# Kernel optimization log

Hardware: AMD Instinct MI355X
Metric: run time of the kernel (lower is better)

## Reference

```python
import jax, jax.numpy as jnp
import numpy as np

S, B, D = 4096, 4, 1024
APERTURE = 256
SCALE = 1.0 / np.sqrt(D)
EPS = 1e-6
NEG_INF = -jnp.inf


def _xavier(key, shape, gain=np.sqrt(2.0)):
    fan_in, fan_out = shape[1], shape[0]
    a = gain * np.sqrt(6.0 / (fan_in + fan_out))
    return jax.random.uniform(key, shape, jnp.float32, -a, a)


def setup_inputs() -> dict:
    key = jax.random.key(0)
    ks = jax.random.split(key, 8)
    return {
        "x": jax.random.normal(ks[0], (S, B, D), jnp.float32),
        "Wk": _xavier(ks[1], (D, D)),
        "Wq": _xavier(ks[2], (D, D)),
        "Wv": _xavier(ks[3], (D, D)),
        "Wp": _xavier(ks[4], (D, D)),
        "W1": _xavier(ks[5], (D, D)),
        "b1": jnp.full((D,), 0.1, jnp.float32),
        "W2": _xavier(ks[6], (1, D)),
        "b2": jnp.full((1,), 0.1, jnp.float32),
        "gamma": jnp.ones((D,), jnp.float32),
        "beta": jnp.zeros((D,), jnp.float32),
    }


def _layer_norm(y, gamma, beta):
    m = jnp.mean(y, axis=-1, keepdims=True)
    v = jnp.mean((y - m) ** 2, axis=-1, keepdims=True)
    return (y - m) * jax.lax.rsqrt(v + EPS) * gamma + beta


def reference(x, Wk, Wq, Wv, Wp, W1, b1, W2, b2, gamma, beta):
    # x: (S, B, D) -> (B, S, D)
    xb = jnp.transpose(x, (1, 0, 2))
    K = jnp.einsum('bsd,ed->bse', xb, Wk)
    Q = jnp.einsum('bsd,ed->bse', xb, Wq)
    V = jnp.einsum('bsd,ed->bse', xb, Wv)
    e = jnp.einsum('bqd,bkd->bqk', Q, K) * SCALE  # (B, S, S)
    # ignore_self: -inf on diagonal
    eye = jnp.eye(S, dtype=bool)
    e = jnp.where(eye[None, :, :], NEG_INF, e)
    # aperture mask: torch masks where tril(e,ap)*triu(e,-ap) == 0
    scope = jnp.tril(e, APERTURE) * jnp.triu(e, -APERTURE)
    e = jnp.where(scope == 0, NEG_INF, e)
    alpha = jax.nn.softmax(e, axis=2)  # dropout is identity at eval
    c = jnp.einsum('bqk,bkd->bqd', alpha, V)
    c = jnp.einsum('bqd,ed->bqe', c, Wp)
    y = c + xb
    y = _layer_norm(y, gamma, beta)
    y = jax.nn.relu(jnp.einsum('bsd,ed->bse', y, W1) + b1)
    y = _layer_norm(y, gamma, beta)
    y = jax.nn.sigmoid(jnp.einsum('bsd,ed->bse', y, W2) + b2)  # (B, S, 1)
    return jnp.transpose(y, (1, 0, 2))  # (S, B, 1)
```

## Files before the change

### kernel.cpp

```cpp
#include <hip/hip_runtime.h>
#include <stdint.h>
#include <math.h>

#define S_LEN 4096
#define BATCH 4
#define DIM   1024
#define AP    256
#define NBLK  32
#define BANDC 640
#define SCALE 0.03125f

typedef __attribute__((ext_vector_type(4))) float f32x4;
typedef __attribute__((ext_vector_type(8))) short bf16x8;

__device__ __forceinline__ ushort f2bf(float f) {
  union { float f; uint32_t u; } v; v.f = f;
  uint32_t r = v.u + 0x7FFFu + ((v.u >> 16) & 1u);
  return (ushort)(r >> 16);
}

__device__ __forceinline__ void gload16(const void* g, void* l) {
  __builtin_amdgcn_global_load_lds((const __attribute__((address_space(1))) void*)g,
                                   (__attribute__((address_space(3))) void*)l,
                                   16, 0, 0);
}

__device__ __forceinline__ float block_sum(float v, float* red) {
  #pragma unroll
  for (int o = 32; o > 0; o >>= 1) v += __shfl_xor(v, o, 64);
  const int w = threadIdx.x >> 6;
  if ((threadIdx.x & 63) == 0) red[w] = v;
  __syncthreads();
  v = red[0] + red[1] + red[2] + red[3];
  __syncthreads();
  return v;
}

__device__ __forceinline__ float block_max(float v, float* red) {
  #pragma unroll
  for (int o = 32; o > 0; o >>= 1) v = fmaxf(v, __shfl_xor(v, o, 64));
  const int w = threadIdx.x >> 6;
  if ((threadIdx.x & 63) == 0) red[w] = v;
  __syncthreads();
  v = fmaxf(fmaxf(red[0], red[1]), fmaxf(red[2], red[3]));
  __syncthreads();
  return v;
}

#define STAGE2(dstbase, g0, g1, kcol) \
  gload16((g0) + (kcol), lds + (dstbase) + stOff); \
  gload16((g1) + (kcol), lds + (dstbase) + 4096 + stOff);

#define MFMA_QUAD(arow, av, bv) \
  __builtin_amdgcn_s_setprio(1); \
  _Pragma("unroll") for (int m = 0; m < 4; ++m) \
  _Pragma("unroll") for (int n = 0; n < 4; ++n) \
    acc[(arow) + m][n] = __builtin_amdgcn_mfma_f32_16x16x32_bf16(av[m], bv[n], acc[(arow) + m][n], 0, 0, 0); \
  __builtin_amdgcn_s_setprio(0);

__device__ __forceinline__ void gemm256_core(
    const ushort* __restrict__ Ablk, int lda,
    const ushort* __restrict__ Bblk, int ldb,
    int K, ushort* __restrict__ lds,
    f32x4 acc[8][4])
{
  const int tid  = threadIdx.x;
  const int lane = tid & 63;
  const int wave = tid >> 6;
  const int wr = wave >> 2;
  const int wn = wave & 3;

  const int srow = tid >> 2;
  const int gseg = (tid & 3) ^ ((tid >> 3) & 3);
  const ushort* gA0 = Ablk + (size_t)srow * lda + gseg * 8;
  const ushort* gA1 = Ablk + (size_t)(srow + 128) * lda + gseg * 8;
  const ushort* gB0 = Bblk + (size_t)srow * ldb + gseg * 8;
  const ushort* gB1 = Bblk + (size_t)(srow + 128) * ldb + gseg * 8;
  const int stOff = wave * 512;

  const int l15 = lane & 15;
  const int seg = (lane >> 4) ^ ((lane >> 1) & 3);
  const int raBase = (wr * 128 + l15) * 32 + seg * 8;
  const int rbBase = (wn * 64  + l15) * 32 + seg * 8;

  const int NT = K >> 6;

  STAGE2(0,     gA0, gA1, 0)
  STAGE2(16384, gB0, gB1, 0)
  STAGE2(8192,  gA0, gA1, 32)
  STAGE2(24576, gB0, gB1, 32)
  asm volatile("s_waitcnt vmcnt(0)" ::: "memory");
  __builtin_amdgcn_s_barrier();

  for (int t = 0; t < NT; ++t) {
    const int rb = (t & 1) * 32768;
    const int sb = ((t + 1) & 1) * 32768;
    const int k1 = (t + 1) << 6;
    const bool more = (t + 1 < NT);

    bf16x8 aA[4], aB[4], bA[4], bB[4];

    #pragma unroll
    for (int m = 0; m < 4; ++m) aA[m] = *(const bf16x8*)(lds + rb + raBase + m * 512);
    #pragma unroll
    for (int n = 0; n < 4; ++n) bA[n] = *(const bf16x8*)(lds + rb + 16384 + rbBase + n * 512);
    #pragma unroll
    for (int m = 0; m < 4; ++m) aB[m] = *(const bf16x8*)(lds + rb + raBase + (m + 4) * 512);
    if (more) {
      STAGE2(sb,         gA0, gA1, k1)
      STAGE2(sb + 16384, gB0, gB1, k1)
    }

    MFMA_QUAD(0, aA, bA)

    #pragma unroll
    for (int m = 0; m < 4; ++m) aA[m] = *(const bf16x8*)(lds + rb + 8192 + raBase + m * 512);
    #pragma unroll
    for (int n = 0; n < 4; ++n) bB[n] = *(const bf16x8*)(lds + rb + 24576 + rbBase + n * 512);
    if (more) {
      STAGE2(sb + 8192,  gA0, gA1, k1 + 32)
      STAGE2(sb + 24576, gB0, gB1, k1 + 32)
    }

    MFMA_QUAD(4, aB, bA)

    #pragma unroll
    for (int m = 0; m < 4; ++m) aB[m] = *(const bf16x8*)(lds + rb + 8192 + raBase + (m + 4) * 512);

    MFMA_QUAD(0, aA, bB)

    MFMA_QUAD(4, aB, bB)

    asm volatile("s_waitcnt vmcnt(0)" ::: "memory");
    __builtin_amdgcn_s_barrier();
  }
}

#define ACC256_ZERO(acc) \
  _Pragma("unroll") for (int m_ = 0; m_ < 8; m_++) \
  _Pragma("unroll") for (int n_ = 0; n_ < 4; n_++) \
  _Pragma("unroll") for (int r_ = 0; r_ < 4; r_++) acc[m_][n_][r_] = 0.0f;

__device__ __forceinline__ void epi256_store_bf16(
    f32x4 acc[8][4], ushort* __restrict__ lds,
    ushort* __restrict__ dst, int rowbase, int colb)
{
  __syncthreads();
  const int lane_ = threadIdx.x & 63;
  const int wave_ = threadIdx.x >> 6;
  const int wrb_ = (wave_ >> 2) * 128;
  const int wnb_ = (wave_ & 3) * 64;
  const int rb_ = (lane_ >> 4) << 2;
  const int cb_ = lane_ & 15;
  #pragma unroll
  for (int m = 0; m < 8; m++)
    #pragma unroll
    for (int n = 0; n < 4; n++)
      #pragma unroll
      for (int r = 0; r < 4; r++) {
        const int rl = wrb_ + m * 16 + rb_ + r;
        const int cl = wnb_ + n * 16 + cb_;
        const int cs = cl ^ (((rl >> 2) & 3) << 4);
        lds[rl * 256 + cs] = f2bf(acc[m][n][r]);
      }
  __syncthreads();
  #pragma unroll
  for (int it = 0; it < 16; ++it) {
    const int chunk = it * 512 + threadIdx.x;
    const int rl = chunk >> 5;
    const int c16 = chunk & 31;
    const int csw = (c16 * 16) ^ (((rl >> 2) & 3) << 5);
    bf16x8 v = *(const bf16x8*)((const char*)lds + rl * 512 + csw);
    *(bf16x8*)(dst + (size_t)(rowbase + rl) * DIM + colb + c16 * 8) = v;
  }
}

#define EPI256_BEGIN(acc) { \
  const int lane_ = threadIdx.x & 63; \
  const int wave_ = threadIdx.x >> 6; \
  const int wrb_ = (wave_ >> 2) * 128; \
  const int wnb_ = (wave_ & 3) * 64; \
  const int rb_ = (lane_ >> 4) << 2; \
  const int cb_ = lane_ & 15; \
  _Pragma("unroll") for (int m_ = 0; m_ < 8; m_++) \
  _Pragma("unroll") for (int n_ = 0; n_ < 4; n_++) \
  _Pragma("unroll") for (int r_ = 0; r_ < 4; r_++) { \
    const int rloc = wrb_ + m_ * 16 + rb_ + r_; \
    const int cloc = wnb_ + n_ * 16 + cb_; \
    const float aval = acc[m_][n_][r_];
#define EPI256_END() } }

__device__ __forceinline__ void gemm_core(
    const ushort* __restrict__ Ablk, int lda,
    const ushort* __restrict__ Bblk, int ldb,
    int k_begin, int k_end,
    ushort* __restrict__ lds,
    f32x4 acc[4][4])
{
  const int tid  = threadIdx.x;
  const int lane = tid & 63;
  const int wr = ((tid >> 7) & 1) * 64;
  const int wc = ((tid >> 6) & 1) * 64;
  const int lr = lane & 15;
  const int seg = (lane >> 4) ^ ((lane >> 1) & 3);

  const int srow = tid >> 2;
  const int gseg = (tid & 3) ^ ((tid >> 3) & 3);
  const ushort* gA0 = Ablk + (size_t)srow * lda + gseg * 8;
  const ushort* gA1 = Ablk + (size_t)(srow + 64) * lda + gseg * 8;
  const ushort* gB0 = Bblk + (size_t)srow * ldb + gseg * 8;
  const ushort* gB1 = Bblk + (size_t)(srow + 64) * ldb + gseg * 8;
  const int stA = (tid >> 6) * 512;

  const int NT = (k_end - k_begin) >> 5;

  gload16(gA0 + k_begin, lds + stA);
  gload16(gA1 + k_begin, lds + 2048 + stA);
  gload16(gB0 + k_begin, lds + 4096 + stA);
  gload16(gB1 + k_begin, lds + 6144 + stA);

  for (int t = 0; t < NT; ++t) {
    if (t + 1 < NT) {
      ushort* buf = lds + ((t + 1) & 1) * 8192;
      const int k0 = k_begin + (t + 1) * 32;
      gload16(gA0 + k0, buf + stA);
      gload16(gA1 + k0, buf + 2048 + stA);
      gload16(gB0 + k0, buf + 4096 + stA);
      gload16(gB1 + k0, buf + 6144 + stA);
      asm volatile("s_waitcnt vmcnt(4)" ::: "memory");
    } else {
      asm volatile("s_waitcnt vmcnt(0)" ::: "memory");
    }
    __builtin_amdgcn_s_barrier();

    const ushort* buf = lds + (t & 1) * 8192;
    bf16x8 af[4], bfv[4];
    #pragma unroll
    for (int m = 0; m < 4; m++)
      af[m] = *(const bf16x8*)(buf + (wr + m * 16 + lr) * 32 + seg * 8);
    #pragma unroll
    for (int n = 0; n < 4; n++)
      bfv[n] = *(const bf16x8*)(buf + 4096 + (wc + n * 16 + lr) * 32 + seg * 8);

    __builtin_amdgcn_s_setprio(1);
    #pragma unroll
    for (int m = 0; m < 4; m++)
      #pragma unroll
      for (int n = 0; n < 4; n++)
        acc[m][n] = __builtin_amdgcn_mfma_f32_16x16x32_bf16(af[m], bfv[n], acc[m][n], 0, 0, 0);
    __builtin_amdgcn_s_setprio(0);
    asm volatile("s_waitcnt lgkmcnt(0)" ::: "memory");
  }
}

#define ACC_ZERO(acc) \
  _Pragma("unroll") for (int m_ = 0; m_ < 4; m_++) \
  _Pragma("unroll") for (int n_ = 0; n_ < 4; n_++) \
  _Pragma("unroll") for (int r_ = 0; r_ < 4; r_++) acc[m_][n_][r_] = 0.0f;

#define EPI_BEGIN(acc) { \
  const int lane_ = threadIdx.x & 63; \
  const int wr_ = ((threadIdx.x >> 7) & 1) * 64; \
  const int wc_ = ((threadIdx.x >> 6) & 1) * 64; \
  const int rb_ = (lane_ >> 4) << 2; \
  const int cb_ = lane_ & 15; \
  _Pragma("unroll") for (int m_ = 0; m_ < 4; m_++) \
  _Pragma("unroll") for (int n_ = 0; n_ < 4; n_++) \
  _Pragma("unroll") for (int r_ = 0; r_ < 4; r_++) { \
    const int rloc = wr_ + m_ * 16 + rb_ + r_; \
    const int cloc = wc_ + n_ * 16 + cb_; \
    const float aval = acc[m_][n_][r_];
#define EPI_END() } }

__global__ __launch_bounds__(256) void prep_x(const float* __restrict__ x, ushort* __restrict__ xb) {
  size_t idx = ((size_t)blockIdx.x * 256 + threadIdx.x) * 4;
  int d = (int)(idx & 1023);
  int s = (int)((idx >> 10) & 4095);
  int b = (int)(idx >> 22);
  float4 v = *(const float4*)(x + ((size_t)s * BATCH + b) * DIM + d);
  ushort4 o;
  o.x = f2bf(v.x); o.y = f2bf(v.y); o.z = f2bf(v.z); o.w = f2bf(v.w);
  *(ushort4*)(xb + idx) = o;
}

__global__ __launch_bounds__(256) void f2bf_all(
    const float* __restrict__ Wk, const float* __restrict__ Wq, const float* __restrict__ Wv,
    const float* __restrict__ Wp, const float* __restrict__ W1,
    ushort* __restrict__ wqkv, ushort* __restrict__ wpb, ushort* __restrict__ w1b)
{
  const int g = blockIdx.x;
  const int which = g >> 10;
  const int idx = ((g & 1023) * 256 + threadIdx.x) * 4;
  const float* src = (which == 0) ? Wk : (which == 1) ? Wq : (which == 2) ? Wv
                   : (which == 3) ? Wp : W1;
  ushort* dst = (which == 0) ? wqkv : (which == 1) ? wqkv + 1048576
              : (which == 2) ? wqkv + 2097152 : (which == 3) ? wpb : w1b;
  float4 v = *(const float4*)(src + idx);
  ushort4 o;
  o.x = f2bf(v.x); o.y = f2bf(v.y); o.z = f2bf(v.z); o.w = f2bf(v.w);
  *(ushort4*)(dst + idx) = o;
}

__global__ __launch_bounds__(512, 2) void qkv_gemm256(
    const ushort* __restrict__ xb, const ushort* __restrict__ wqkv,
    ushort* __restrict__ Kp, ushort* __restrict__ Qp, ushort* __restrict__ Vp)
{
  __shared__ ushort lds[65536];
  const int nid = (blockIdx.x & 7) * 96 + (blockIdx.x >> 3);
  const int by = nid / 12;
  const int bx = nid % 12;
  f32x4 acc[8][4];
  ACC256_ZERO(acc)
  gemm256_core(xb + (size_t)by * 256 * DIM, DIM,
               wqkv + (size_t)bx * 256 * DIM, DIM, DIM, lds, acc);
  ushort* dst = (bx < 4) ? Kp : (bx < 8) ? Qp : Vp;
  epi256_store_bf16(acc, lds, dst, by * 256, (bx & 3) * 256);
}

__global__ __launch_bounds__(512, 2) void wp_gemm256(
    const ushort* __restrict__ cbuf, const ushort* __restrict__ wpb,
    const float* __restrict__ x, float* __restrict__ y0)
{
  __shared__ ushort lds[65536];
  const int nid = (blockIdx.x & 7) * 32 + (blockIdx.x >> 3);
  const int by = nid >> 2;
  const int bx = nid & 3;
  f32x4 acc[8][4];
  ACC256_ZERO(acc)
  gemm256_core(cbuf + (size_t)by * 256 * DIM, DIM,
               wpb + (size_t)bx * 256 * DIM, DIM, DIM, lds, acc);
  EPI256_BEGIN(acc)
    int row = by * 256 + rloc;
    int col = bx * 256 + cloc;
    int b = row >> 12, s = row & 4095;
    y0[(size_t)row * DIM + col] = aval + x[((size_t)s * BATCH + b) * DIM + col];
  EPI256_END()
}

__global__ __launch_bounds__(512, 2) void ffn1_gemm256(
    const ushort* __restrict__ y1, const ushort* __restrict__ w1b,
    const float* __restrict__ b1, float* __restrict__ h0)
{
  __shared__ ushort lds[65536];
  const int nid = (blockIdx.x & 7) * 32 + (blockIdx.x >> 3);
  const int by = nid >> 2;
  const int bx = nid & 3;
  f32x4 acc[8][4];
  ACC256_ZERO(acc)
  gemm256_core(y1 + (size_t)by * 256 * DIM, DIM,
               w1b + (size_t)bx * 256 * DIM, DIM, DIM, lds, acc);
  EPI256_BEGIN(acc)
    int row = by * 256 + rloc;
    int col = bx * 256 + cloc;
    h0[(size_t)row * DIM + col] = fmaxf(aval + b1[col], 0.0f);
  EPI256_END()
}

__global__ __launch_bounds__(256) void transpose_v(const ushort* __restrict__ V, ushort* __restrict__ VT) {
  __shared__ ushort tile[64][66];
  const int s0 = blockIdx.x * 64, d0 = blockIdx.y * 64, b = blockIdx.z;
  const ushort* Vb = V + (size_t)b * S_LEN * DIM;
  ushort* VTb = VT + (size_t)b * DIM * S_LEN;
  #pragma unroll
  for (int it = 0; it < 16; it++) {
    int flat = it * 256 + threadIdx.x;
    int r = flat >> 6, c = flat & 63;
    tile[r][c] = Vb[(size_t)(s0 + r) * DIM + d0 + c];
  }
  __syncthreads();
  #pragma unroll
  for (int it = 0; it < 16; it++) {
    int flat = it * 256 + threadIdx.x;
    int r = flat >> 6, c = flat & 63;
    VTb[(size_t)(d0 + r) * S_LEN + s0 + c] = tile[c][r];
  }
}

__global__ __launch_bounds__(256) void scores_gemm(
    const ushort* __restrict__ Qp, const ushort* __restrict__ Kp,
    float* __restrict__ eband)
{
  const int nid = (blockIdx.x & 7) * 80 + (blockIdx.x >> 3);
  const int b   = nid / 160;
  const int rem = nid % 160;
  const int i   = rem / 5;
  const int jj  = rem % 5;
  const int j   = i - 2 + jj;
  if (j < 0 || j >= NBLK) return;
  __shared__ ushort lds[16384];
  f32x4 acc[4][4];
  ACC_ZERO(acc)
  gemm_core(Qp + ((size_t)b * S_LEN + i * 128) * DIM, DIM,
            Kp + ((size_t)b * S_LEN + j * 128) * DIM, DIM, 0, DIM, lds, acc);
  EPI_BEGIN(acc)
    int q = i * 128 + rloc;
    int k = j * 128 + cloc;
    float v = aval * SCALE;
    int dqk = q - k;
    if (dqk == 0 || dqk > AP || dqk < -AP) v = -INFINITY;
    eband[((size_t)b * S_LEN + q) * BANDC + jj * 128 + cloc] = v;
  EPI_END()
}

__global__ __launch_bounds__(256) void softmax_band(const float* __restrict__ eband,
                                                    ushort* __restrict__ aband)
{
  __shared__ float red[4];
  const int qg = blockIdx.x;
  const int s  = qg & 4095;
  const int i  = s >> 7;
  const float* row = eband + (size_t)qg * BANDC;
  ushort* arow = aband + (size_t)qg * BANDC;

  float vals[3];
  bool  valid[3];
  float mx = -INFINITY;
  #pragma unroll
  for (int t = 0; t < 3; t++) {
    int idx = threadIdx.x + t * 256;
    int jj = idx >> 7;
    int j = i - 2 + jj;
    bool ok = (idx < BANDC) && (j >= 0) && (j < NBLK);
    valid[t] = ok;
    float v = ok ? row[idx] : -INFINITY;
    vals[t] = v;
    mx = fmaxf(mx, v);
  }
  float bmax = block_max(mx, red);
  float ss = 0.0f;
  #pragma unroll
  for (int t = 0; t < 3; t++) {
    float e = valid[t] ? __expf(vals[t] - bmax) : 0.0f;
    vals[t] = e;
    ss += e;
  }
  float inv = 1.0f / block_sum(ss, red);
  #pragma unroll
  for (int t = 0; t < 3; t++) {
    int idx = threadIdx.x + t * 256;
    if (idx < BANDC) arow[idx] = f2bf(vals[t] * inv);
  }
}

__global__ __launch_bounds__(256) void av_gemm(
    const ushort* __restrict__ aband, const ushort* __restrict__ VT,
    ushort* __restrict__ cbuf)
{
  const int nid = (blockIdx.x & 7) * 128 + (blockIdx.x >> 3);
  const int by = nid >> 3;
  const int b = by >> 5, i = by & 31;
  const int bx = nid & 7;
  const int jj_lo = (i < 2) ? (2 - i) : 0;
  const int jj_hi = (i > 29) ? (34 - i) : 5;
  __shared__ ushort lds[16384];
  f32x4 acc[4][4];
  ACC_ZERO(acc)
  const ushort* Ablk = aband + ((size_t)b * S_LEN + i * 128) * BANDC;
  const ushort* Bblk = VT + (size_t)b * DIM * S_LEN + (size_t)bx * 128 * S_LEN + (i - 2) * 128;
  gemm_core(Ablk, BANDC, Bblk, S_LEN, jj_lo * 128, jj_hi * 128, lds, acc);

  __syncthreads();
  {
    const int lane_ = threadIdx.x & 63;
    const int wr_ = ((threadIdx.x >> 7) & 1) * 64;
    const int wc_ = ((threadIdx.x >> 6) & 1) * 64;
    const int rb_ = (lane_ >> 4) << 2;
    const int cb_ = lane_ & 15;
    #pragma unroll
    for (int m = 0; m < 4; m++)
      #pragma unroll
      for (int n = 0; n < 4; n++)
        #pragma unroll
        for (int r = 0; r < 4; r++) {
          const int rl = wr_ + m * 16 + rb_ + r;
          const int cl = wc_ + n * 16 + cb_;
          const int cs = cl ^ (((rl >> 2) & 3) << 4);
          lds[rl * 128 + cs] = f2bf(acc[m][n][r]);
        }
  }
  __syncthreads();
  ushort* dst = cbuf + ((size_t)b * S_LEN + i * 128) * DIM + bx * 128;
  #pragma unroll
  for (int it = 0; it < 8; ++it) {
    const int chunk = it * 256 + threadIdx.x;
    const int rl = chunk >> 4;
    const int c16 = chunk & 15;
    const int csw = (c16 * 16) ^ (((rl >> 2) & 3) << 5);
    bf16x8 v = *(const bf16x8*)((const char*)lds + rl * 256 + csw);
    *(bf16x8*)(dst + (size_t)rl * DIM + c16 * 8) = v;
  }
}

__global__ __launch_bounds__(256) void ln_kernel(const float* __restrict__ y0, ushort* __restrict__ y1,
                                                 const float* __restrict__ gamma, const float* __restrict__ beta)
{
  __shared__ float red[4];
  const size_t q = blockIdx.x;
  const float* row = y0 + q * DIM;
  float v[4];
  #pragma unroll
  for (int t = 0; t < 4; t++) v[t] = row[threadIdx.x + t * 256];
  float mean = block_sum(v[0] + v[1] + v[2] + v[3], red) * (1.0f / DIM);
  float q2 = 0.0f;
  #pragma unroll
  for (int t = 0; t < 4; t++) { float d = v[t] - mean; q2 += d * d; }
  float var = block_sum(q2, red) * (1.0f / DIM);
  float rstd = rsqrtf(var + 1e-6f);
  #pragma unroll
  for (int t = 0; t < 4; t++) {
    int d = threadIdx.x + t * 256;
    y1[q * DIM + d] = f2bf((v[t] - mean) * rstd * gamma[d] + beta[d]);
  }
}

__global__ __launch_bounds__(256) void head_kernel(const float* __restrict__ h0,
    const float* __restrict__ gamma, const float* __restrict__ beta,
    const float* __restrict__ W2, const float* __restrict__ b2,
    float* __restrict__ out)
{
  __shared__ float red[4];
  const int qg = blockIdx.x;
  const int b = qg >> 12, s = qg & 4095;
  const float* row = h0 + (size_t)qg * DIM;
  float v[4];
  #pragma unroll
  for (int t = 0; t < 4; t++) v[t] = row[threadIdx.x + t * 256];
  float mean = block_sum(v[0] + v[1] + v[2] + v[3], red) * (1.0f / DIM);
  float q2 = 0.0f;
  #pragma unroll
  for (int t = 0; t < 4; t++) { float d = v[t] - mean; q2 += d * d; }
  float var = block_sum(q2, red) * (1.0f / DIM);
  float rstd = rsqrtf(var + 1e-6f);
  float part = 0.0f;
  #pragma unroll
  for (int t = 0; t < 4; t++) {
    int d = threadIdx.x + t * 256;
    part += ((v[t] - mean) * rstd * gamma[d] + beta[d]) * W2[d];
  }
  float logit = block_sum(part, red) + b2[0];
  if (threadIdx.x == 0) out[(size_t)s * BATCH + b] = 1.0f / (1.0f + expf(-logit));
}

extern "C" void kernel_launch(void* const* d_in, const int* in_sizes, int n_in,
                              void* d_out, int out_size, void* d_ws, size_t ws_size,
                              hipStream_t stream) {
  const float* x     = (const float*)d_in[0];
  const float* Wk    = (const float*)d_in[1];
  const float* Wq    = (const float*)d_in[2];
  const float* Wv    = (const float*)d_in[3];
  const float* Wp    = (const float*)d_in[4];
  const float* W1    = (const float*)d_in[5];
  const float* b1    = (const float*)d_in[6];
  const float* W2    = (const float*)d_in[7];
  const float* b2    = (const float*)d_in[8];
  const float* gamma = (const float*)d_in[9];
  const float* beta  = (const float*)d_in[10];
  float* out = (float*)d_out;

  char* w = (char*)d_ws;
  ushort* xb   = (ushort*)(w + 0);
  ushort* wqkv = (ushort*)(w + 33554432);
  ushort* wpb  = (ushort*)(w + 39845888);
  ushort* w1b  = (ushort*)(w + 41943040);
  ushort* Qp   = (ushort*)(w + 44040192);
  ushort* Kp   = (ushort*)(w + 77594624);
  ushort* Vp   = (ushort*)(w + 111149056);
  ushort* VT   = (ushort*)(w + 144703488);
  float*  big  = (float*)(w + 178257920);
  ushort* aband = Qp;
  ushort* cbuf  = Kp;
  ushort* y1    = Vp;
  float* eband = big;
  float* y0    = big;
  float* h0    = big;

  prep_x<<<16384, 256, 0, stream>>>(x, xb);
  f2bf_all<<<5120, 256, 0, stream>>>(Wk, Wq, Wv, Wp, W1, wqkv, wpb, w1b);

  qkv_gemm256<<<768, 512, 0, stream>>>(xb, wqkv, Kp, Qp, Vp);
  transpose_v<<<dim3(64, 16, 4), 256, 0, stream>>>(Vp, VT);
  scores_gemm<<<640, 256, 0, stream>>>(Qp, Kp, eband);
  softmax_band<<<16384, 256, 0, stream>>>(eband, aband);
  av_gemm<<<1024, 256, 0, stream>>>(aband, VT, cbuf);
  wp_gemm256<<<256, 512, 0, stream>>>(cbuf, wpb, x, y0);
  ln_kernel<<<16384, 256, 0, stream>>>(y0, y1, gamma, beta);
  ffn1_gemm256<<<256, 512, 0, stream>>>(y1, w1b, b1, h0);
  head_kernel<<<16384, 256, 0, stream>>>(h0, gamma, beta, W2, b2, out);
}
```

Before: 376.2 us.

## Restructure GEMM core into barrier-phased pipeline, store FFN1 output as bf16, vectorize LN

The shared 256x256 GEMM core now preloads the first fragments before the loop, uses partial vmcnt waits and sched barriers, and splits each K step into four barrier-separated phases so LDS reads, global-to-LDS staging and MFMAs overlap more. The FFN1 epilogue writes a bias+ReLU bf16 tile through LDS with coalesced stores instead of fp32 scattered stores, and the head kernel reads bf16. The LN and head kernels use vector float4/ushort4 loads. The bf16 hidden state lowers precision before the final layer norm, and the extra barriers and partial waits carry ordering risk.

```diff
diff --git a/kernel.cpp b/kernel.cpp
--- a/kernel.cpp
+++ b/kernel.cpp
@@ -18,6 +18,9 @@
   uint32_t r = v.u + 0x7FFFu + ((v.u >> 16) & 1u);
   return (ushort)(r >> 16);
 }
+__device__ __forceinline__ float bf2f(ushort u) {
+  union { uint32_t u; float f; } v; v.u = ((uint32_t)u) << 16; return v.f;
+}
 
 __device__ __forceinline__ void gload16(const void* g, void* l) {
   __builtin_amdgcn_global_load_lds((const __attribute__((address_space(1))) void*)g,
@@ -51,12 +54,16 @@
   gload16((g0) + (kcol), lds + (dstbase) + stOff); \
   gload16((g1) + (kcol), lds + (dstbase) + 4096 + stOff);
 
-#define MFMA_QUAD(arow, av, bv) \
+#define MFMA16(arow, av, bv) \
   __builtin_amdgcn_s_setprio(1); \
   _Pragma("unroll") for (int m = 0; m < 4; ++m) \
   _Pragma("unroll") for (int n = 0; n < 4; ++n) \
     acc[(arow) + m][n] = __builtin_amdgcn_mfma_f32_16x16x32_bf16(av[m], bv[n], acc[(arow) + m][n], 0, 0, 0); \
   __builtin_amdgcn_s_setprio(0);
+
+#define PHASE_CUT() \
+  __builtin_amdgcn_sched_barrier(0); \
+  asm volatile("s_barrier" ::: "memory");
 
 __device__ __forceinline__ void gemm256_core(
     const ushort* __restrict__ Ablk, int lda,
@@ -89,50 +96,57 @@
   STAGE2(16384, gB0, gB1, 0)
   STAGE2(8192,  gA0, gA1, 32)
   STAGE2(24576, gB0, gB1, 32)
-  asm volatile("s_waitcnt vmcnt(0)" ::: "memory");
-  __builtin_amdgcn_s_barrier();
+  asm volatile("s_waitcnt vmcnt(4)" ::: "memory");
+  asm volatile("s_barrier" ::: "memory");
+
+  bf16x8 aE[4], aO[4], bE[4], bO[4];
+  #pragma unroll
+  for (int m = 0; m < 4; ++m) aE[m] = *(const bf16x8*)(lds + raBase + m * 512);
+  #pragma unroll
+  for (int n = 0; n < 4; ++n) bE[n] = *(const bf16x8*)(lds + 16384 + rbBase + n * 512);
 
   for (int t = 0; t < NT; ++t) {
     const int rb = (t & 1) * 32768;
-    const int sb = ((t + 1) & 1) * 32768;
+    const int sb = rb ^ 32768;
     const int k1 = (t + 1) << 6;
     const bool more = (t + 1 < NT);
 
-    bf16x8 aA[4], aB[4], bA[4], bB[4];
-
-    #pragma unroll
-    for (int m = 0; m < 4; ++m) aA[m] = *(const bf16x8*)(lds + rb + raBase + m * 512);
-    #pragma unroll
-    for (int n = 0; n < 4; ++n) bA[n] = *(const bf16x8*)(lds + rb + 16384 + rbBase + n * 512);
-    #pragma unroll
-    for (int m = 0; m < 4; ++m) aB[m] = *(const bf16x8*)(lds + rb + raBase + (m + 4) * 512);
+    #pragma unroll
+    for (int m = 0; m < 4; ++m) aO[m] = *(const bf16x8*)(lds + rb + raBase + (m + 4) * 512);
     if (more) {
       STAGE2(sb,         gA0, gA1, k1)
       STAGE2(sb + 16384, gB0, gB1, k1)
     }
-
-    MFMA_QUAD(0, aA, bA)
-
-    #pragma unroll
-    for (int m = 0; m < 4; ++m) aA[m] = *(const bf16x8*)(lds + rb + 8192 + raBase + m * 512);
-    #pragma unroll
-    for (int n = 0; n < 4; ++n) bB[n] = *(const bf16x8*)(lds + rb + 24576 + rbBase + n * 512);
+    MFMA16(0, aE, bE)
+    if (more) asm volatile("s_waitcnt vmcnt(4)" ::: "memory");
+    else      asm volatile("s_waitcnt vmcnt(0)" ::: "memory");
+    PHASE_CUT()
+
+    #pragma unroll
+    for (int m = 0; m < 4; ++m) aE[m] = *(const bf16x8*)(lds + rb + 8192 + raBase + m * 512);
+    #pragma unroll
+    for (int n = 0; n < 4; ++n) bO[n] = *(const bf16x8*)(lds + rb + 24576 + rbBase + n * 512);
     if (more) {
       STAGE2(sb + 8192,  gA0, gA1, k1 + 32)
       STAGE2(sb + 24576, gB0, gB1, k1 + 32)
     }
-
-    MFMA_QUAD(4, aB, bA)
-
-    #pragma unroll
-    for (int m = 0; m < 4; ++m) aB[m] = *(const bf16x8*)(lds + rb + 8192 + raBase + (m + 4) * 512);
-
-    MFMA_QUAD(0, aA, bB)
-
-    MFMA_QUAD(4, aB, bB)
-
-    asm volatile("s_waitcnt vmcnt(0)" ::: "memory");
-    __builtin_amdgcn_s_barrier();
+    MFMA16(4, aO, bE)
+    PHASE_CUT()
+
+    #pragma unroll
+    for (int m = 0; m < 4; ++m) aO[m] = *(const bf16x8*)(lds + rb + 8192 + raBase + (m + 4) * 512);
+    MFMA16(0, aE, bO)
+    if (more) asm volatile("s_waitcnt vmcnt(4)" ::: "memory");
+    PHASE_CUT()
+
+    if (more) {
+      #pragma unroll
+      for (int m = 0; m < 4; ++m) aE[m] = *(const bf16x8*)(lds + sb + raBase + m * 512);
+      #pragma unroll
+      for (int n = 0; n < 4; ++n) bE[n] = *(const bf16x8*)(lds + sb + 16384 + rbBase + n * 512);
+    }
+    MFMA16(4, aO, bO)
+    PHASE_CUT()
   }
 }
 
@@ -163,6 +177,43 @@
         const int cs = cl ^ (((rl >> 2) & 3) << 4);
         lds[rl * 256 + cs] = f2bf(acc[m][n][r]);
       }
+  __syncthreads();
+  #pragma unroll
+  for (int it = 0; it < 16; ++it) {
+    const int chunk = it * 512 + threadIdx.x;
+    const int rl = chunk >> 5;
+    const int c16 = chunk & 31;
+    const int csw = (c16 * 16) ^ (((rl >> 2) & 3) << 5);
+    bf16x8 v = *(const bf16x8*)((const char*)lds + rl * 512 + csw);
+    *(bf16x8*)(dst + (size_t)(rowbase + rl) * DIM + colb + c16 * 8) = v;
+  }
+}
+
+__device__ __forceinline__ void epi256_store_relu_bf16(
+    f32x4 acc[8][4], ushort* __restrict__ lds,
+    ushort* __restrict__ dst, int rowbase, int colb,
+    const float* __restrict__ bias)
+{
+  __syncthreads();
+  const int lane_ = threadIdx.x & 63;
+  const int wave_ = threadIdx.x >> 6;
+  const int wrb_ = (wave_ >> 2) * 128;
+  const int wnb_ = (wave_ & 3) * 64;
+  const int rb_ = (lane_ >> 4) << 2;
+  const int cb_ = lane_ & 15;
+  #pragma unroll
+  for (int m = 0; m < 8; m++)
+    #pragma unroll
+    for (int n = 0; n < 4; n++) {
+      const int cl = wnb_ + n * 16 + cb_;
+      const float bv = bias[colb + cl];
+      #pragma unroll
+      for (int r = 0; r < 4; r++) {
+        const int rl = wrb_ + m * 16 + rb_ + r;
+        const int cs = cl ^ (((rl >> 2) & 3) << 4);
+        lds[rl * 256 + cs] = f2bf(fmaxf(acc[m][n][r] + bv, 0.0f));
+      }
+    }
   __syncthreads();
   #pragma unroll
   for (int it = 0; it < 16; ++it) {
@@ -339,7 +390,7 @@
 
 __global__ __launch_bounds__(512, 2) void ffn1_gemm256(
     const ushort* __restrict__ y1, const ushort* __restrict__ w1b,
-    const float* __restrict__ b1, float* __restrict__ h0)
+    const float* __restrict__ b1, ushort* __restrict__ h0)
 {
   __shared__ ushort lds[65536];
   const int nid = (blockIdx.x & 7) * 32 + (blockIdx.x >> 3);
@@ -349,11 +400,7 @@
   ACC256_ZERO(acc)
   gemm256_core(y1 + (size_t)by * 256 * DIM, DIM,
                w1b + (size_t)bx * 256 * DIM, DIM, DIM, lds, acc);
-  EPI256_BEGIN(acc)
-    int row = by * 256 + rloc;
-    int col = bx * 256 + cloc;
-    h0[(size_t)row * DIM + col] = fmaxf(aval + b1[col], 0.0f);
-  EPI256_END()
+  epi256_store_relu_bf16(acc, lds, h0, by * 256, bx * 256, b1);
 }
 
 __global__ __launch_bounds__(256) void transpose_v(const ushort* __restrict__ V, ushort* __restrict__ VT) {
@@ -496,24 +543,24 @@
 {
   __shared__ float red[4];
   const size_t q = blockIdx.x;
-  const float* row = y0 + q * DIM;
-  float v[4];
-  #pragma unroll
-  for (int t = 0; t < 4; t++) v[t] = row[threadIdx.x + t * 256];
-  float mean = block_sum(v[0] + v[1] + v[2] + v[3], red) * (1.0f / DIM);
-  float q2 = 0.0f;
-  #pragma unroll
-  for (int t = 0; t < 4; t++) { float d = v[t] - mean; q2 += d * d; }
+  const int d0 = threadIdx.x * 4;
+  float4 v = *(const float4*)(y0 + q * DIM + d0);
+  float mean = block_sum(v.x + v.y + v.z + v.w, red) * (1.0f / DIM);
+  float q2 = (v.x - mean) * (v.x - mean) + (v.y - mean) * (v.y - mean)
+           + (v.z - mean) * (v.z - mean) + (v.w - mean) * (v.w - mean);
   float var = block_sum(q2, red) * (1.0f / DIM);
   float rstd = rsqrtf(var + 1e-6f);
-  #pragma unroll
-  for (int t = 0; t < 4; t++) {
-    int d = threadIdx.x + t * 256;
-    y1[q * DIM + d] = f2bf((v[t] - mean) * rstd * gamma[d] + beta[d]);
-  }
-}
-
-__global__ __launch_bounds__(256) void head_kernel(const float* __restrict__ h0,
+  float4 g = *(const float4*)(gamma + d0);
+  float4 bb = *(const float4*)(beta + d0);
+  ushort4 o;
+  o.x = f2bf((v.x - mean) * rstd * g.x + bb.x);
+  o.y = f2bf((v.y - mean) * rstd * g.y + bb.y);
+  o.z = f2bf((v.z - mean) * rstd * g.z + bb.z);
+  o.w = f2bf((v.w - mean) * rstd * g.w + bb.w);
+  *(ushort4*)(y1 + q * DIM + d0) = o;
+}
+
+__global__ __launch_bounds__(256) void head_kernel(const ushort* __restrict__ h0,
     const float* __restrict__ gamma, const float* __restrict__ beta,
     const float* __restrict__ W2, const float* __restrict__ b2,
     float* __restrict__ out)
@@ -521,22 +568,21 @@
   __shared__ float red[4];
   const int qg = blockIdx.x;
   const int b = qg >> 12, s = qg & 4095;
-  const float* row = h0 + (size_t)qg * DIM;
-  float v[4];
-  #pragma unroll
-  for (int t = 0; t < 4; t++) v[t] = row[threadIdx.x + t * 256];
-  float mean = block_sum(v[0] + v[1] + v[2] + v[3], red) * (1.0f / DIM);
-  float q2 = 0.0f;
-  #pragma unroll
-  for (int t = 0; t < 4; t++) { float d = v[t] - mean; q2 += d * d; }
+  const int d0 = threadIdx.x * 4;
+  ushort4 u = *(const ushort4*)(h0 + (size_t)qg * DIM + d0);
+  float v0 = bf2f(u.x), v1 = bf2f(u.y), v2 = bf2f(u.z), v3 = bf2f(u.w);
+  float mean = block_sum(v0 + v1 + v2 + v3, red) * (1.0f / DIM);
+  float q2 = (v0 - mean) * (v0 - mean) + (v1 - mean) * (v1 - mean)
+           + (v2 - mean) * (v2 - mean) + (v3 - mean) * (v3 - mean);
   float var = block_sum(q2, red) * (1.0f / DIM);
   float rstd = rsqrtf(var + 1e-6f);
-  float part = 0.0f;
-  #pragma unroll
-  for (int t = 0; t < 4; t++) {
-    int d = threadIdx.x + t * 256;
-    part += ((v[t] - mean) * rstd * gamma[d] + beta[d]) * W2[d];
-  }
+  float4 g = *(const float4*)(gamma + d0);
+  float4 bb = *(const float4*)(beta + d0);
+  float4 w2 = *(const float4*)(W2 + d0);
+  float part = ((v0 - mean) * rstd * g.x + bb.x) * w2.x
+             + ((v1 - mean) * rstd * g.y + bb.y) * w2.y
+             + ((v2 - mean) * rstd * g.z + bb.z) * w2.z
+             + ((v3 - mean) * rstd * g.w + bb.w) * w2.w;
   float logit = block_sum(part, red) + b2[0];
   if (threadIdx.x == 0) out[(size_t)s * BATCH + b] = 1.0f / (1.0f + expf(-logit));
 }
@@ -570,9 +616,9 @@
   ushort* aband = Qp;
   ushort* cbuf  = Kp;
   ushort* y1    = Vp;
+  ushort* h0    = xb;
   float* eband = big;
   float* y0    = big;
-  float* h0    = big;
 
   prep_x<<<16384, 256, 0, stream>>>(x, xb);
   f2bf_all<<<5120, 256, 0, stream>>>(Wk, Wq, Wv, Wp, W1, wqkv, wpb, w1b);
```

New measurement: 373.5 us. No clear change (-0.7%).
